# Kernel optimization log

Measured on AMD Instinct MI355X. Metric: run time of the kernel, lower is better.

Reference implementation:

```python
import jax, jax.numpy as jnp
import numpy as np

B, C, H, W = 2, 128, 64, 64
D_STATE = 16
EXPAND = 2
D_INNER = C * EXPAND          # 256
DT_RANK = -(-C // 16)         # 8
K = 4                         # scan directions
COMPRESS = 3
SQUEEZE = 30
EPS = 1e-5


def layernorm(x, g, b):
    mu = x.mean(-1, keepdims=True)
    xm = x - mu
    var = (xm * xm).mean(-1, keepdims=True)
    return xm * jax.lax.rsqrt(var + EPS) * g + b


def conv2d(x, w, bias, pad):
    y = jax.lax.conv_general_dilated(x, w, (1, 1), ((pad, pad), (pad, pad)),
                                     dimension_numbers=('NCHW', 'OIHW', 'NCHW'))
    return y + bias[None, :, None, None]


def selective_scan(xs, dts, A, Bs, Cs):
    # xs,dts: (B,K,D,L); A: (K,D,N); Bs,Cs: (B,K,N,L)
    dt_t = jnp.moveaxis(dts, -1, 0)
    x_t = jnp.moveaxis(xs, -1, 0)
    B_t = jnp.moveaxis(Bs, -1, 0)
    C_t = jnp.moveaxis(Cs, -1, 0)
    h0 = jnp.zeros(xs.shape[:3] + (A.shape[-1],), xs.dtype)

    def step(h, inp):
        dt_l, x_l, b_l, c_l = inp          # (B,K,D),(B,K,D),(B,K,N),(B,K,N)
        dA = jnp.exp(dt_l[..., None] * A)  # (B,K,D,N)
        h = dA * h + (dt_l * x_l)[..., None] * b_l[:, :, None, :]
        y = jnp.einsum('bkdn,bkn->bkd', h, c_l)
        return h, y

    _, ys = jax.lax.scan(step, h0, (dt_t, x_t, B_t, C_t))
    return jnp.moveaxis(ys, 0, -1)  # (B,K,D,L)


def ss2d(x, p):  # x: (B,H,W,C) -> (B,H,W,C)
    xz = x @ p['in_proj_w'].T
    xc, z = jnp.split(xz, 2, axis=-1)
    xc = xc.transpose(0, 3, 1, 2)  # (B,D,H,W)
    xc = jax.lax.conv_general_dilated(xc, p['conv_w'], (1, 1), ((1, 1), (1, 1)),
                                      feature_group_count=D_INNER,
                                      dimension_numbers=('NCHW', 'OIHW', 'NCHW'))
    xc = jax.nn.silu(xc + p['conv_b'][None, :, None, None])
    b, d, h, w = xc.shape
    L = h * w
    x_hw = xc.reshape(b, d, L)
    x_wh = xc.transpose(0, 1, 3, 2).reshape(b, d, L)
    xs = jnp.stack([x_hw, x_wh, x_hw[..., ::-1], x_wh[..., ::-1]], axis=1)  # (B,4,D,L)
    x_dbl = jnp.einsum('bkdl,kcd->bkcl', xs, p['x_proj_w'])
    dtr, Bs, Cs = jnp.split(x_dbl, [DT_RANK, DT_RANK + D_STATE], axis=2)
    dts = jnp.einsum('bkrl,kdr->bkdl', dtr, p['dt_w'])
    dts = jax.nn.softplus(dts + p['dt_b'][None, :, :, None])
    A = -jnp.exp(p['A_logs']).reshape(K, d, D_STATE)
    ys = selective_scan(xs, dts, A, Bs, Cs)
    ys = ys + xs * p['Ds'].reshape(K, d)[None, :, :, None]
    inv = ys[:, 2:4][..., ::-1]  # undo flipped scans
    wh = lambda t: t.reshape(b, d, w, h).transpose(0, 1, 3, 2).reshape(b, d, L)
    y = ys[:, 0] + inv[:, 0] + wh(ys[:, 1]) + wh(inv[:, 1])
    y = y.transpose(0, 2, 1).reshape(b, h, w, d)
    y = layernorm(y, p['out_norm_g'], p['out_norm_b'])
    y = y * jax.nn.silu(z)
    return y @ p['out_proj_w'].T


def cab(x, p):  # x: (B,C,H,W)
    t = jax.nn.gelu(conv2d(x, p['cab_w1'], p['cab_b1'], 1), approximate=False)
    t = conv2d(t, p['cab_w2'], p['cab_b2'], 1)
    s = t.mean((2, 3), keepdims=True)
    s = jax.nn.relu(conv2d(s, p['ca_w1'], p['ca_b1'], 0))
    s = jax.nn.sigmoid(conv2d(s, p['ca_w2'], p['ca_b2'], 0))
    return t * s


def vss_block(input, p):
    inp = input.transpose(0, 2, 3, 1)  # (B,H,W,C)
    x = inp * p['skip_scale'] + ss2d(layernorm(inp, p['ln1_g'], p['ln1_b']), p)
    c = cab(layernorm(x, p['ln2_g'], p['ln2_b']).transpose(0, 3, 1, 2), p)
    x = x * p['skip_scale2'] + c.transpose(0, 2, 3, 1)
    return x.transpose(0, 3, 1, 2)


def setup_inputs() -> dict:
    key = jax.random.key(0)
    ks = jax.random.split(key, 16)
    rn = lambda i, shp, s=0.02: jax.random.normal(ks[i], shp, jnp.float32) * s
    return {
        'input': jax.random.normal(ks[0], (B, C, H, W), jnp.float32),
        'ln1_g': jnp.ones((C,), jnp.float32), 'ln1_b': jnp.zeros((C,), jnp.float32),
        'skip_scale': jnp.ones((C,), jnp.float32), 'skip_scale2': jnp.ones((C,), jnp.float32),
        'ln2_g': jnp.ones((C,), jnp.float32), 'ln2_b': jnp.zeros((C,), jnp.float32),
        'in_proj_w': rn(1, (2 * D_INNER, C)),
        'conv_w': rn(2, (D_INNER, 1, 3, 3), 0.1),
        'conv_b': jnp.zeros((D_INNER,), jnp.float32),
        'x_proj_w': rn(3, (K, DT_RANK + 2 * D_STATE, D_INNER)),
        'dt_w': rn(4, (K, D_INNER, DT_RANK), 0.1),
        'dt_b': rn(5, (K, D_INNER), 0.1),
        'A_logs': jnp.log(jnp.tile(jnp.arange(1, D_STATE + 1, dtype=jnp.float32), (K * D_INNER, 1))),
        'Ds': jnp.ones((K * D_INNER,), jnp.float32),
        'out_norm_g': jnp.ones((D_INNER,), jnp.float32), 'out_norm_b': jnp.zeros((D_INNER,), jnp.float32),
        'out_proj_w': rn(6, (C, D_INNER)),
        'cab_w1': rn(7, (C // COMPRESS, C, 3, 3), 0.05),
        'cab_b1': jnp.zeros((C // COMPRESS,), jnp.float32),
        'cab_w2': rn(8, (C, C // COMPRESS, 3, 3), 0.05),
        'cab_b2': jnp.zeros((C,), jnp.float32),
        'ca_w1': rn(9, (C // SQUEEZE, C, 1, 1), 0.05),
        'ca_b1': jnp.zeros((C // SQUEEZE,), jnp.float32),
        'ca_w2': rn(10, (C, C // SQUEEZE, 1, 1), 0.05),
        'ca_b2': jnp.zeros((C,), jnp.float32),
    }


def reference(input, ln1_g, ln1_b, skip_scale, skip_scale2, ln2_g, ln2_b,
              in_proj_w, conv_w, conv_b, x_proj_w, dt_w, dt_b, A_logs, Ds,
              out_norm_g, out_norm_b, out_proj_w,
              cab_w1, cab_b1, cab_w2, cab_b2, ca_w1, ca_b1, ca_w2, ca_b2):
    p = dict(ln1_g=ln1_g, ln1_b=ln1_b, skip_scale=skip_scale, skip_scale2=skip_scale2,
             ln2_g=ln2_g, ln2_b=ln2_b, in_proj_w=in_proj_w, conv_w=conv_w, conv_b=conv_b,
             x_proj_w=x_proj_w, dt_w=dt_w, dt_b=dt_b, A_logs=A_logs, Ds=Ds,
             out_norm_g=out_norm_g, out_norm_b=out_norm_b, out_proj_w=out_proj_w,
             cab_w1=cab_w1, cab_b1=cab_b1, cab_w2=cab_w2, cab_b2=cab_b2,
             ca_w1=ca_w1, ca_b1=ca_b1, ca_w2=ca_w2, ca_b2=ca_b2)
    return vss_block(input, p)
```

## Files before the change

kernel.cpp:

```cpp
#include <hip/hip_runtime.h>
#include <math.h>

#define BB 2
#define CC 128
#define HH 64
#define WW 64
#define LL 4096
#define DI 256
#define NS 16
#define KK 4
#define OC1 42

#define NC 256
#define CL 16

#define K3_POS 16
#define BCW 48

__device__ __forceinline__ float sigmoidf_(float x) { return 1.f / (1.f + __expf(-x)); }
__device__ __forceinline__ float siluf_(float x)    { return x * sigmoidf_(x); }

__device__ __forceinline__ int scan_pos(int k, int i) {
  if (k == 0) return i;
  if (k == 1) return ((i & 63) << 6) | (i >> 6);
  if (k == 2) return (LL - 1) - i;
  int j = (LL - 1) - i;
  return ((j & 63) << 6) | (j >> 6);
}

__global__ __launch_bounds__(256) void k1_ln_inproj(
    const float* __restrict__ inp, const float* __restrict__ g, const float* __restrict__ b,
    const float* __restrict__ wproj, float* __restrict__ xcin, float* __restrict__ zbuf) {
  __shared__ float sx[64][132];
  __shared__ float sw[128][68];
  __shared__ float smu[64], srs[64];
  const int tid = threadIdx.x;
  const int rt = blockIdx.x & 3;
  const int pt = blockIdx.x >> 2;
  const int bb = pt >> 6;
  const int pbase = (pt & 63) << 6;

  for (int idx = tid; idx < 64 * CC; idx += 256) {
    int c = idx >> 6, pl = idx & 63;
    sx[pl][c] = inp[((size_t)bb * CC + c) * LL + pbase + pl];
  }
  __syncthreads();
  {
    int pl = tid >> 2, j = tid & 3;
    float s = 0.f, s2 = 0.f;
    for (int c = j; c < CC; c += 4) { float v = sx[pl][c]; s += v; s2 += v * v; }
    s += __shfl_xor(s, 1); s2 += __shfl_xor(s2, 1);
    s += __shfl_xor(s, 2); s2 += __shfl_xor(s2, 2);
    if (j == 0) {
      float mu = s * (1.f / CC);
      smu[pl] = mu;
      srs[pl] = rsqrtf(s2 * (1.f / CC) - mu * mu + 1e-5f);
    }
  }
  __syncthreads();
  for (int idx = tid; idx < 64 * CC; idx += 256) {
    int c = idx & 127, pl = idx >> 7;
    sx[pl][c] = (sx[pl][c] - smu[pl]) * srs[pl] * g[c] + b[c];
  }

  const int pg = tid & 7, rg = tid >> 3;
  float acc[8][4];
#pragma unroll
  for (int j = 0; j < 8; j++)
#pragma unroll
    for (int q = 0; q < 4; q++) acc[j][q] = 0.f;

  for (int kc = 0; kc < CC; kc += 64) {
    __syncthreads();
    for (int idx = tid; idx < 128 * 64; idx += 256) {
      int cl = idx & 63, rl = idx >> 6;
      sw[rl][cl] = wproj[(size_t)(rt * 128 + rl) * CC + kc + cl];
    }
    __syncthreads();
#pragma unroll 4
    for (int i = 0; i < 16; i++) {
      const int k0 = kc + 4 * i, kl0 = 4 * i;
      float4 xv[8], wv[4];
#pragma unroll
      for (int j = 0; j < 8; j++) xv[j] = *(const float4*)&sx[pg + 8 * j][k0];
#pragma unroll
      for (int q = 0; q < 4; q++) wv[q] = *(const float4*)&sw[rg + 32 * q][kl0];
#pragma unroll
      for (int j = 0; j < 8; j++)
#pragma unroll
        for (int q = 0; q < 4; q++) {
          acc[j][q] += xv[j].x * wv[q].x + xv[j].y * wv[q].y
                     + xv[j].z * wv[q].z + xv[j].w * wv[q].w;
        }
    }
  }

  float* buf = (rt < 2) ? xcin : zbuf;
  const int drow = (rt & 1) * 128;
#pragma unroll
  for (int j = 0; j < 8; j++) {
    const int p = pbase + pg + 8 * j;
    float* dst = buf + ((size_t)bb * LL + p) * DI + drow;
#pragma unroll
    for (int q = 0; q < 4; q++) dst[rg + 32 * q] = acc[j][q];
  }
}

__global__ __launch_bounds__(256) void k2_dwconv(
    const float* __restrict__ xcin, const float* __restrict__ cw, const float* __restrict__ cb,
    float* __restrict__ xconv) {
  const int w0 = (blockIdx.x & 7) * 8;
  const int hh = (blockIdx.x >> 3) & 63;
  const int bb = blockIdx.x >> 9;
  const int d = threadIdx.x;

  float wv[9];
#pragma unroll
  for (int kk = 0; kk < 9; kk++) wv[kk] = cw[d * 9 + kk];
  const float bias = cb[d];

  float xin[3][10];
#pragma unroll
  for (int kh = 0; kh < 3; kh++) {
    int r = hh + kh - 1;
    bool vr = (r >= 0 && r < HH);
#pragma unroll
    for (int c = 0; c < 10; c++) {
      int cc2 = w0 + c - 1;
      bool vc = (cc2 >= 0 && cc2 < WW);
      xin[kh][c] = (vr && vc) ? xcin[((size_t)bb * LL + r * WW + cc2) * DI + d] : 0.f;
    }
  }
#pragma unroll
  for (int j = 0; j < 8; j++) {
    float acc = bias;
#pragma unroll
    for (int kh = 0; kh < 3; kh++)
#pragma unroll
      for (int kw = 0; kw < 3; kw++)
        acc += wv[kh * 3 + kw] * xin[kh][j + kw];
    xconv[((size_t)bb * LL + hh * WW + w0 + j) * DI + d] = siluf_(acc);
  }
}

__global__ __launch_bounds__(256) void k3_proj(
    const float* __restrict__ xconv, const float* __restrict__ xpw,
    float* __restrict__ BCbuf) {
  __shared__ float sx[16][68];
  __shared__ float sw[160][68];
  const int tid = threadIdx.x;
  const int bb = blockIdx.x >> 8;
  const int pbase = (blockIdx.x & 255) << 4;

  const int pg = tid & 7, rb = tid >> 3;
  float acc[2][5];
#pragma unroll
  for (int j = 0; j < 2; j++)
#pragma unroll
    for (int q = 0; q < 5; q++) acc[j][q] = 0.f;

  for (int kc = 0; kc < DI; kc += 64) {
    __syncthreads();
    for (int idx = tid; idx < 16 * 64; idx += 256) {
      int cl = idx & 63, pl = idx >> 6;
      sx[pl][cl] = xconv[((size_t)bb * LL + pbase + pl) * DI + kc + cl];
    }
    for (int idx = tid; idx < 160 * 64; idx += 256) {
      int cl = idx & 63, rl = idx >> 6;
      sw[rl][cl] = xpw[(size_t)rl * DI + kc + cl];
    }
    __syncthreads();
#pragma unroll 4
    for (int i = 0; i < 16; i++) {
      float4 xv[2], wv[5];
#pragma unroll
      for (int j = 0; j < 2; j++) xv[j] = *(const float4*)&sx[2 * pg + j][4 * i];
#pragma unroll
      for (int q = 0; q < 5; q++) wv[q] = *(const float4*)&sw[rb + 32 * q][4 * i];
#pragma unroll
      for (int j = 0; j < 2; j++)
#pragma unroll
        for (int q = 0; q < 5; q++) {
          acc[j][q] += xv[j].x * wv[q].x + xv[j].y * wv[q].y
                     + xv[j].z * wv[q].z + xv[j].w * wv[q].w;
        }
    }
  }

#pragma unroll
  for (int j = 0; j < 2; j++) {
    const int p = pbase + 2 * pg + j;
#pragma unroll
    for (int q = 0; q < 5; q++) {
      const int r = rb + 32 * q;
      const int k = r / 40, c0 = r - k * 40;
      BCbuf[((size_t)(bb * KK + k) * LL + p) * BCW + c0] = acc[j][q];
    }
  }
}

__global__ __launch_bounds__(256) void k4a_chunk(
    const float* __restrict__ xconv, const float* __restrict__ BCbuf,
    const float* __restrict__ A_logs, const float* __restrict__ dtw,
    const float* __restrict__ dtb,
    float* __restrict__ csA, float* __restrict__ csB) {
  __shared__ float sBC[CL][26];
  const int d = threadIdx.x;
  const int chunk = blockIdx.x & (NC - 1);
  const int t = blockIdx.x / NC;
  const int k = t & 3;
  const int bb = t >> 2;
  const int bk = bb * KK + k;
  const int base = chunk * CL;

  for (int idx = d; idx < CL * 24; idx += 256) {
    int ii = idx / 24, j = idx - ii * 24;
    int pos = scan_pos(k, base + ii);
    sBC[ii][j] = BCbuf[((size_t)bk * LL + pos) * BCW + j];
  }
  float a[NS];
  bool fast = true;
#pragma unroll
  for (int n = 0; n < NS; n++) {
    a[n] = -__expf(A_logs[((size_t)k * DI + d) * NS + n]);
    fast = fast && (fabsf(a[n] + (float)(n + 1)) < 1e-3f * (n + 1));
  }
  const float* wdt = dtw + ((size_t)k * DI + d) * 8;
  const float4 wd0 = *(const float4*)wdt;
  const float4 wd1 = *(const float4*)(wdt + 4);
  const float bdt = dtb[k * DI + d];
  __syncthreads();

  const float* x_p = xconv + (size_t)bb * LL * DI + d;

  float Ap[NS], Bc[NS];
#pragma unroll
  for (int n = 0; n < NS; n++) { Ap[n] = 1.f; Bc[n] = 0.f; }

  if (fast) {
    float sumdt = 0.f;
#pragma unroll
    for (int half = 0; half < CL / 8; half++) {
      float xvr[8];
#pragma unroll
      for (int j = 0; j < 8; j++)
        xvr[j] = x_p[(size_t)scan_pos(k, base + half * 8 + j) * DI];
#pragma unroll
      for (int j = 0; j < 8; j++) {
        const int ii = half * 8 + j;
        const float* dr = sBC[ii];
        float u = bdt + wd0.x * dr[0] + wd0.y * dr[1] + wd0.z * dr[2] + wd0.w * dr[3]
                      + wd1.x * dr[4] + wd1.y * dr[5] + wd1.z * dr[6] + wd1.w * dr[7];
        float t2 = __expf(u);
        float E = __builtin_amdgcn_rcpf(1.f + t2);
        float dt = u > 20.f ? u : -0.69314718056f * __log2f(E);
        sumdt += dt;
        float dtx = dt * xvr[j];
        float E2 = E * E;
        float dA1 = E, dA2 = E2;
#pragma unroll
        for (int n = 0; n < NS; n += 2) {
          Bc[n] = dA1 * Bc[n] + dtx * sBC[ii][8 + n];
          Bc[n + 1] = dA2 * Bc[n + 1] + dtx * sBC[ii][9 + n];
          dA1 *= E2; dA2 *= E2;
        }
      }
    }
    float Et = __expf(-sumdt);
    float p = Et;
#pragma unroll
    for (int n = 0; n < NS; n++) { Ap[n] = p; p *= Et; }
  } else {
#pragma unroll 2
    for (int ii = 0; ii < CL; ii++) {
      int pos = scan_pos(k, base + ii);
      float xv = x_p[(size_t)pos * DI];
      const float* dr = sBC[ii];
      float u = bdt + wd0.x * dr[0] + wd0.y * dr[1] + wd0.z * dr[2] + wd0.w * dr[3]
                    + wd1.x * dr[4] + wd1.y * dr[5] + wd1.z * dr[6] + wd1.w * dr[7];
      float t2 = __expf(u);
      float dt = u > 20.f ? u : log1pf(t2);
      float dtx = dt * xv;
#pragma unroll
      for (int n = 0; n < NS; n++) {
        float dA = __expf(dt * a[n]);
        Ap[n] *= dA;
        Bc[n] = dA * Bc[n] + dtx * sBC[ii][8 + n];
      }
    }
  }
  size_t e = ((size_t)(bk * NC + chunk) * NS) * DI + d;
#pragma unroll
  for (int n = 0; n < NS; n++) {
    csA[e + (size_t)n * DI] = Ap[n];
    csB[e + (size_t)n * DI] = Bc[n];
  }
}

__global__ __launch_bounds__(256) void k4b_scanchunks(
    float* csAh, const float* __restrict__ csB) {
  const int d = threadIdx.x;
  const int n = blockIdx.x & (NS - 1);
  const int bk = blockIdx.x >> 4;
  const size_t stride = (size_t)NS * DI;
  size_t e = ((size_t)bk * NC * NS + n) * DI + d;
  float H = 0.f;
  for (int c0 = 0; c0 < NC; c0 += 16) {
    float A[16], Bv[16];
#pragma unroll
    for (int j = 0; j < 16; j++) {
      A[j]  = csAh[e + (size_t)j * stride];
      Bv[j] = csB[e + (size_t)j * stride];
    }
#pragma unroll
    for (int j = 0; j < 16; j++) {
      csAh[e + (size_t)j * stride] = H;
      H = A[j] * H + Bv[j];
    }
    e += (size_t)16 * stride;
  }
}

__global__ __launch_bounds__(256) void k4c_scan(
    const float* __restrict__ xconv, const float* __restrict__ BCbuf,
    const float* __restrict__ A_logs, const float* __restrict__ dtw,
    const float* __restrict__ dtb, const float* __restrict__ Ds,
    const float* __restrict__ hin, float* __restrict__ ys) {
  __shared__ float sBC[CL][BCW];
  const int d = threadIdx.x;
  const int chunk = blockIdx.x & (NC - 1);
  const int t = blockIdx.x / NC;
  const int k = t & 3;
  const int bb = t >> 2;
  const int bk = bb * KK + k;
  const int base = chunk * CL;

  for (int idx = d; idx < CL * 40; idx += 256) {
    int ii = idx / 40, j = idx - ii * 40;
    int pos = scan_pos(k, base + ii);
    sBC[ii][j] = BCbuf[((size_t)bk * LL + pos) * BCW + j];
  }
  float a[NS], h[NS];
  bool fast = true;
  const size_t eh = ((size_t)(bk * NC + chunk) * NS) * DI + d;
#pragma unroll
  for (int n = 0; n < NS; n++) {
    a[n] = -__expf(A_logs[((size_t)k * DI + d) * NS + n]);
    fast = fast && (fabsf(a[n] + (float)(n + 1)) < 1e-3f * (n + 1));
    h[n] = hin[eh + (size_t)n * DI];
  }
  const float* wdt = dtw + ((size_t)k * DI + d) * 8;
  const float4 wd0 = *(const float4*)wdt;
  const float4 wd1 = *(const float4*)(wdt + 4);
  const float bdt = dtb[k * DI + d];
  const float Dd = Ds[k * DI + d];
  __syncthreads();

  const float* x_p = xconv + (size_t)bb * LL * DI + d;
  float* ys_p = ys + (size_t)bk * LL * DI + d;

  if (fast) {
#pragma unroll
    for (int half = 0; half < CL / 8; half++) {
      float xvr[8];
#pragma unroll
      for (int j = 0; j < 8; j++)
        xvr[j] = x_p[(size_t)scan_pos(k, base + half * 8 + j) * DI];
#pragma unroll
      for (int j = 0; j < 8; j++) {
        const int ii = half * 8 + j;
        const float* dr = sBC[ii];
        float u = bdt + wd0.x * dr[0] + wd0.y * dr[1] + wd0.z * dr[2] + wd0.w * dr[3]
                      + wd1.x * dr[4] + wd1.y * dr[5] + wd1.z * dr[6] + wd1.w * dr[7];
        float t2 = __expf(u);
        float E = __builtin_amdgcn_rcpf(1.f + t2);
        float dt = u > 20.f ? u : -0.69314718056f * __log2f(E);
        float dtx = dt * xvr[j];
        float y = xvr[j] * Dd;
        float E2 = E * E;
        float dA1 = E, dA2 = E2;
#pragma unroll
        for (int n = 0; n < NS; n += 2) {
          h[n] = dA1 * h[n] + dtx * sBC[ii][8 + n];
          y += h[n] * sBC[ii][24 + n];
          h[n + 1] = dA2 * h[n + 1] + dtx * sBC[ii][9 + n];
          y += h[n + 1] * sBC[ii][25 + n];
          dA1 *= E2; dA2 *= E2;
        }
        ys_p[(size_t)scan_pos(k, base + ii) * DI] = y;
      }
    }
  } else {
#pragma unroll 2
    for (int ii = 0; ii < CL; ii++) {
      int pos = scan_pos(k, base + ii);
      float xv = x_p[(size_t)pos * DI];
      const float* dr = sBC[ii];
      float u = bdt + wd0.x * dr[0] + wd0.y * dr[1] + wd0.z * dr[2] + wd0.w * dr[3]
                    + wd1.x * dr[4] + wd1.y * dr[5] + wd1.z * dr[6] + wd1.w * dr[7];
      float t2 = __expf(u);
      float dt = u > 20.f ? u : log1pf(t2);
      float dtx = dt * xv;
      float y = xv * Dd;
#pragma unroll
      for (int n = 0; n < NS; n++) {
        float dA = __expf(dt * a[n]);
        h[n] = dA * h[n] + dtx * sBC[ii][8 + n];
        y += h[n] * sBC[ii][24 + n];
      }
      ys_p[(size_t)pos * DI] = y;
    }
  }
}

__global__ __launch_bounds__(256) void k5a_act(
    const float* __restrict__ ys, const float* __restrict__ zbuf,
    const float* __restrict__ ong, const float* __restrict__ onb,
    float* __restrict__ yact) {
  __shared__ float sy[8][260];
  __shared__ float smu[8], srs[8];
  const int tid = threadIdx.x;
  const int bb = blockIdx.x >> 9;
  const int pbase = (blockIdx.x & 511) << 3;

  for (int idx = tid; idx < 8 * DI; idx += 256) {
    int d = idx & 255, pl = idx >> 8;
    size_t o0 = (((size_t)bb * KK + 0) * LL + pbase + pl) * DI + d;
    const size_t st = (size_t)LL * DI;
    sy[pl][d] = ys[o0] + ys[o0 + st] + ys[o0 + 2 * st] + ys[o0 + 3 * st];
  }
  __syncthreads();
  {
    int pl = tid >> 5, j = tid & 31;
    float s = 0.f, s2 = 0.f;
    for (int d = j; d < DI; d += 32) { float v = sy[pl][d]; s += v; s2 += v * v; }
#pragma unroll
    for (int m = 1; m < 32; m <<= 1) { s += __shfl_xor(s, m); s2 += __shfl_xor(s2, m); }
    if (j == 0) {
      float mu = s * (1.f / DI);
      smu[pl] = mu;
      srs[pl] = rsqrtf(s2 * (1.f / DI) - mu * mu + 1e-5f);
    }
  }
  __syncthreads();
  for (int idx = tid; idx < 8 * DI; idx += 256) {
    int d = idx & 255, pl = idx >> 8;
    float zv = zbuf[((size_t)bb * LL + pbase + pl) * DI + d];
    yact[((size_t)bb * LL + pbase + pl) * DI + d] =
        ((sy[pl][d] - smu[pl]) * srs[pl] * ong[d] + onb[d]) * siluf_(zv);
  }
}

__global__ __launch_bounds__(256) void k5b_proj(
    const float* __restrict__ yact, const float* __restrict__ opw,
    const float* __restrict__ inp, const float* __restrict__ sk,
    const float* __restrict__ g2, const float* __restrict__ b2,
    float* __restrict__ xres, float* __restrict__ ln2) {
  __shared__ float sx[16][68];
  __shared__ float sw[128][68];
  __shared__ float sr[16][132];
  __shared__ float smu[16], srs[16];
  const int tid = threadIdx.x;
  const int bb = blockIdx.x >> 8;
  const int pbase = (blockIdx.x & 255) << 4;

  const int pg = tid & 7, rb = tid >> 3;
  float acc[2][4];
#pragma unroll
  for (int j = 0; j < 2; j++)
#pragma unroll
    for (int q = 0; q < 4; q++) acc[j][q] = 0.f;

  for (int kc = 0; kc < DI; kc += 64) {
    __syncthreads();
    for (int idx = tid; idx < 16 * 64; idx += 256) {
      int cl = idx & 63, pl = idx >> 6;
      sx[pl][cl] = yact[((size_t)bb * LL + pbase + pl) * DI + kc + cl];
    }
    for (int idx = tid; idx < 128 * 64; idx += 256) {
      int cl = idx & 63, rl = idx >> 6;
      sw[rl][cl] = opw[(size_t)rl * DI + kc + cl];
    }
    __syncthreads();
#pragma unroll 4
    for (int i = 0; i < 16; i++) {
      float4 xv[2], wv[4];
#pragma unroll
      for (int j = 0; j < 2; j++) xv[j] = *(const float4*)&sx[2 * pg + j][4 * i];
#pragma unroll
      for (int q = 0; q < 4; q++) wv[q] = *(const float4*)&sw[rb + 32 * q][4 * i];
#pragma unroll
      for (int j = 0; j < 2; j++)
#pragma unroll
        for (int q = 0; q < 4; q++) {
          acc[j][q] += xv[j].x * wv[q].x + xv[j].y * wv[q].y
                     + xv[j].z * wv[q].z + xv[j].w * wv[q].w;
        }
    }
  }

#pragma unroll
  for (int j = 0; j < 2; j++) {
    const int p = pbase + 2 * pg + j;
#pragma unroll
    for (int q = 0; q < 4; q++) {
      const int c = rb + 32 * q;
      float r = inp[((size_t)bb * CC + c) * LL + p] * sk[c] + acc[j][q];
      xres[((size_t)bb * LL + p) * CC + c] = r;
      sr[2 * pg + j][c] = r;
    }
  }
  __syncthreads();
  {
    int pl = tid >> 4, jj = tid & 15;
    float s = 0.f, s2 = 0.f;
    for (int c = jj; c < CC; c += 16) { float v = sr[pl][c]; s += v; s2 += v * v; }
#pragma unroll
    for (int m = 1; m < 16; m <<= 1) { s += __shfl_xor(s, m); s2 += __shfl_xor(s2, m); }
    if (jj == 0) {
      float mu = s * (1.f / CC);
      smu[pl] = mu;
      srs[pl] = rsqrtf(s2 * (1.f / CC) - mu * mu + 1e-5f);
    }
  }
  __syncthreads();
  for (int idx = tid; idx < 16 * CC; idx += 256) {
    int pl = idx & 15, c = idx >> 4;
    ln2[((size_t)bb * CC + c) * LL + pbase + pl] =
        (sr[pl][c] - smu[pl]) * srs[pl] * g2[c] + b2[c];
  }
}

__global__ __launch_bounds__(256) void k6a_conv1(
    const float* __restrict__ ln2, const float* __restrict__ w1,
    float* __restrict__ pc1) {
  __shared__ float sIn[16][6][68];
  __shared__ float sw[16 * 9 * OC1];
  const int tid = threadIdx.x;
  const int icq = blockIdx.x & 7;
  const int h4  = (blockIdx.x >> 3) & 15;
  const int bb  = blockIdx.x >> 7;
  const int icb = icq * 16;

  for (int idx = tid; idx < 16 * 6 * 66; idx += 256) {
    int i = idx / 396, rem = idx % 396;
    int rr = rem / 66, j = rem % 66;
    int r = h4 * 4 + rr - 1, c2 = j - 1;
    float v = 0.f;
    if (r >= 0 && r < HH && c2 >= 0 && c2 < WW)
      v = ln2[((size_t)bb * CC + icb + i) * LL + r * WW + c2];
    sIn[i][rr][j] = v;
  }
  for (int idx = tid; idx < OC1 * 16 * 9; idx += 256) {
    int oc = idx / 144, rem = idx % 144;
    int i = rem / 9, kk = rem % 9;
    sw[(i * 9 + kk) * OC1 + oc] = w1[((size_t)oc * CC + icb + i) * 9 + kk];
  }
  __syncthreads();

  const int wq = tid & 7, hq = (tid >> 3) & 3, ocg = tid >> 5;
  float acc[6][8];
#pragma unroll
  for (int q = 0; q < 6; q++)
#pragma unroll
    for (int ww = 0; ww < 8; ww++) acc[q][ww] = 0.f;

  for (int i = 0; i < 16; i++) {
    float xin[3][10];
#pragma unroll
    for (int kh = 0; kh < 3; kh++)
#pragma unroll
      for (int j = 0; j < 10; j++) xin[kh][j] = sIn[i][hq + kh][wq * 8 + j];
#pragma unroll
    for (int q = 0; q < 6; q++) {
      int oc = ocg + 8 * q;
      if (oc >= OC1) break;
      float wv[9];
#pragma unroll
      for (int kk = 0; kk < 9; kk++) wv[kk] = sw[(i * 9 + kk) * OC1 + oc];
#pragma unroll
      for (int kh = 0; kh < 3; kh++)
#pragma unroll
        for (int kw = 0; kw < 3; kw++)
#pragma unroll
          for (int ww = 0; ww < 8; ww++)
            acc[q][ww] += wv[kh * 3 + kw] * xin[kh][ww + kw];
    }
  }

  const int hrow = h4 * 4 + hq;
#pragma unroll
  for (int q = 0; q < 6; q++) {
    int oc = ocg + 8 * q;
    if (oc >= OC1) break;
    float* dst = pc1 + (((size_t)icq * BB + bb) * OC1 + oc) * LL + hrow * WW + wq * 8;
    *(float4*)dst       = make_float4(acc[q][0], acc[q][1], acc[q][2], acc[q][3]);
    *(float4*)(dst + 4) = make_float4(acc[q][4], acc[q][5], acc[q][6], acc[q][7]);
  }
}

__global__ __launch_bounds__(256) void k6b_reduce(
    const float* __restrict__ pc1, const float* __restrict__ b1,
    float* __restrict__ t1) {
  const int oc = blockIdx.x % OC1;
  const int bb = blockIdx.x / OC1;
  const float bias = b1[oc];
  const size_t st = (size_t)BB * OC1 * LL;
  const float* src = pc1 + ((size_t)bb * OC1 + oc) * LL;
  float* dst = t1 + ((size_t)bb * OC1 + oc) * LL;
  for (int i = threadIdx.x; i < LL / 4; i += 256) {
    float4 s = ((const float4*)src)[i];
#pragma unroll
    for (int icq = 1; icq < 8; icq++) {
      float4 v = *(const float4*)(src + (size_t)icq * st + i * 4);
      s.x += v.x; s.y += v.y; s.z += v.z; s.w += v.w;
    }
    float r[4] = {s.x + bias, s.y + bias, s.z + bias, s.w + bias};
#pragma unroll
    for (int q = 0; q < 4; q++)
      r[q] = 0.5f * r[q] * (1.f + erff(r[q] * 0.70710678118654752f));
    ((float4*)dst)[i] = make_float4(r[0], r[1], r[2], r[3]);
  }
}

__global__ __launch_bounds__(256) void k7_conv2(
    const float* __restrict__ t1, const float* __restrict__ w2,
    float* __restrict__ pc2) {
  __shared__ float sIn[21][4][68];
  __shared__ float swT[32 * 196];
  const int tid = threadIdx.x;
  const int icq = blockIdx.x & 1;
  const int h2  = (blockIdx.x >> 1) & 31;
  const int ocq = (blockIdx.x >> 6) & 3;
  const int bb  = blockIdx.x >> 8;
  const int icb = icq * 21;

  for (int idx = tid; idx < 21 * 4 * 66; idx += 256) {
    int i = idx / 264, rem = idx % 264;
    int rr = rem / 66, j = rem % 66;
    int r = h2 * 2 + rr - 1, c2 = j - 1;
    float v = 0.f;
    if (r >= 0 && r < HH && c2 >= 0 && c2 < WW)
      v = t1[((size_t)bb * OC1 + icb + i) * LL + r * WW + c2];
    sIn[i][rr][j] = v;
  }
  for (int idx = tid; idx < 32 * 189; idx += 256) {
    int ol = idx / 189, ikk = idx % 189;
    swT[ol * 196 + ikk] = w2[(size_t)(ocq * 32 + ol) * (OC1 * 9) + icb * 9 + ikk];
  }
  __syncthreads();

  const int wq = tid & 7, hq = (tid >> 3) & 1, ocg = tid >> 4;
  float acc[2][8];
#pragma unroll
  for (int q = 0; q < 2; q++)
#pragma unroll
    for (int ww = 0; ww < 8; ww++) acc[q][ww] = 0.f;

  for (int i = 0; i < 21; i++) {
    float xin[3][10];
#pragma unroll
    for (int kh = 0; kh < 3; kh++)
#pragma unroll
      for (int j = 0; j < 10; j++) xin[kh][j] = sIn[i][hq + kh][wq * 8 + j];
#pragma unroll
    for (int q = 0; q < 2; q++) {
      int ol = ocg + 16 * q;
      float wv[9];
#pragma unroll
      for (int kk = 0; kk < 9; kk++) wv[kk] = swT[ol * 196 + i * 9 + kk];
#pragma unroll
      for (int kh = 0; kh < 3; kh++)
#pragma unroll
        for (int kw = 0; kw < 3; kw++)
#pragma unroll
          for (int ww = 0; ww < 8; ww++)
            acc[q][ww] += wv[kh * 3 + kw] * xin[kh][ww + kw];
    }
  }

  const int hrow = h2 * 2 + hq;
#pragma unroll
  for (int q = 0; q < 2; q++) {
    int oc = ocq * 32 + ocg + 16 * q;
    float* dst = pc2 + (((size_t)icq * BB + bb) * CC + oc) * LL + hrow * WW + wq * 8;
    *(float4*)dst       = make_float4(acc[q][0], acc[q][1], acc[q][2], acc[q][3]);
    *(float4*)(dst + 4) = make_float4(acc[q][4], acc[q][5], acc[q][6], acc[q][7]);
  }
}

__global__ __launch_bounds__(256) void k8_mean(
    const float* __restrict__ pc2, const float* __restrict__ b2,
    float* __restrict__ t2, float* __restrict__ smean) {
  __shared__ float red[4];
  const int bc = blockIdx.x;
  const int bb = bc >> 7, c = bc & 127;
  const float bias = b2[c];
  const size_t st = (size_t)BB * CC * LL;
  const float* src = pc2 + ((size_t)bb * CC + c) * LL;
  float* dst = t2 + (size_t)bc * LL;
  float s = 0.f;
  for (int i = threadIdx.x; i < LL / 4; i += 256) {
    float4 v0 = ((const float4*)src)[i];
    float4 v1 = *(const float4*)(src + st + i * 4);
    float4 r = make_float4(v0.x + v1.x + bias, v0.y + v1.y + bias,
                           v0.z + v1.z + bias, v0.w + v1.w + bias);
    ((float4*)dst)[i] = r;
    s += r.x + r.y + r.z + r.w;
  }
#pragma unroll
  for (int m = 1; m < 64; m <<= 1) s += __shfl_xor(s, m);
  if ((threadIdx.x & 63) == 0) red[threadIdx.x >> 6] = s;
  __syncthreads();
  if (threadIdx.x == 0) smean[bc] = (red[0] + red[1] + red[2] + red[3]) * (1.f / LL);
}

__global__ __launch_bounds__(256) void k10_final(
    const float* __restrict__ xres, const float* __restrict__ t2,
    const float* __restrict__ smean,
    const float* __restrict__ cw1, const float* __restrict__ cb1,
    const float* __restrict__ cw2, const float* __restrict__ cb2,
    const float* __restrict__ sk2, float* __restrict__ out) {
  __shared__ float mid[4];
  const int tid = threadIdx.x;
  const int bc = blockIdx.x;
  const int bb = bc >> 7, c = bc & 127;

  {
    const int wv = tid >> 6, ln = tid & 63;
    float s = cw1[wv * CC + ln] * smean[bb * CC + ln]
            + cw1[wv * CC + 64 + ln] * smean[bb * CC + 64 + ln];
#pragma unroll
    for (int m = 1; m < 64; m <<= 1) s += __shfl_xor(s, m);
    if (ln == 0) mid[wv] = fmaxf(s + cb1[wv], 0.f);
  }
  __syncthreads();
  float a = cb2[c];
#pragma unroll
  for (int m = 0; m < 4; m++) a += cw2[c * 4 + m] * mid[m];
  const float sv = sigmoidf_(a);

  const float ss = sk2[c];
  const float* t2r = t2 + (size_t)bc * LL;
  float* outr = out + (size_t)bc * LL;
  for (int i = tid; i < LL; i += 256)
    outr[i] = xres[((size_t)bb * LL + i) * CC + c] * ss + t2r[i] * sv;
}


extern "C" void kernel_launch(void* const* d_in, const int* in_sizes, int n_in,
                              void* d_out, int out_size, void* d_ws, size_t ws_size,
                              hipStream_t stream) {
  const float* input      = (const float*)d_in[0];
  const float* ln1_g      = (const float*)d_in[1];
  const float* ln1_b      = (const float*)d_in[2];
  const float* skip_scale = (const float*)d_in[3];
  const float* skip_scale2= (const float*)d_in[4];
  const float* ln2_g      = (const float*)d_in[5];
  const float* ln2_b      = (const float*)d_in[6];
  const float* in_proj_w  = (const float*)d_in[7];
  const float* conv_w     = (const float*)d_in[8];
  const float* conv_b     = (const float*)d_in[9];
  const float* x_proj_w   = (const float*)d_in[10];
  const float* dt_w       = (const float*)d_in[11];
  const float* dt_b       = (const float*)d_in[12];
  const float* A_logs     = (const float*)d_in[13];
  const float* Ds         = (const float*)d_in[14];
  const float* out_norm_g = (const float*)d_in[15];
  const float* out_norm_b = (const float*)d_in[16];
  const float* out_proj_w = (const float*)d_in[17];
  const float* cab_w1     = (const float*)d_in[18];
  const float* cab_b1     = (const float*)d_in[19];
  const float* cab_w2     = (const float*)d_in[20];
  const float* cab_b2     = (const float*)d_in[21];
  const float* ca_w1      = (const float*)d_in[22];
  const float* ca_b1      = (const float*)d_in[23];
  const float* ca_w2      = (const float*)d_in[24];
  const float* ca_b2      = (const float*)d_in[25];

  float* ws = (float*)d_ws;
  float* xcin  = ws;
  float* zbuf  = xcin + (size_t)BB * LL * DI;
  float* xconv = zbuf + (size_t)BB * LL * DI;
  float* BCbuf = xconv + (size_t)BB * LL * DI;
  float* ysb   = BCbuf + (size_t)BB * KK * LL * BCW;
  float* xres  = ysb + (size_t)BB * KK * LL * DI;
  float* ln2b  = xres + (size_t)BB * LL * CC;
  float* t1b   = ln2b + (size_t)BB * CC * LL;
  float* t2b   = t1b + (size_t)BB * OC1 * LL;
  float* smean = t2b + (size_t)BB * CC * LL;
  float* csA   = smean + BB * CC;
  float* csB   = ysb;
  float* pc1   = ysb;
  float* yact  = csA;
  float* pc2   = ysb + (size_t)3 * 1024 * 1024;

  k1_ln_inproj<<<512, 256, 0, stream>>>(input, ln1_g, ln1_b, in_proj_w, xcin, zbuf);
  k2_dwconv<<<BB * HH * (WW / 8), 256, 0, stream>>>(xcin, conv_w, conv_b, xconv);
  k3_proj<<<BB * (LL / K3_POS), 256, 0, stream>>>(xconv, x_proj_w, BCbuf);
  k4a_chunk<<<BB * KK * NC, 256, 0, stream>>>(xconv, BCbuf, A_logs, dt_w, dt_b, csA, csB);
  k4b_scanchunks<<<BB * KK * NS, 256, 0, stream>>>(csA, csB);
  k4c_scan<<<BB * KK * NC, 256, 0, stream>>>(xconv, BCbuf, A_logs, dt_w, dt_b, Ds, csA, ysb);
  k5a_act<<<BB * (LL / 8), 256, 0, stream>>>(ysb, zbuf, out_norm_g, out_norm_b, yact);
  k5b_proj<<<BB * (LL / 16), 256, 0, stream>>>(yact, out_proj_w, input, skip_scale,
                                               ln2_g, ln2_b, xres, ln2b);
  k6a_conv1<<<BB * 16 * 8, 256, 0, stream>>>(ln2b, cab_w1, pc1);
  k6b_reduce<<<BB * OC1, 256, 0, stream>>>(pc1, cab_b1, t1b);
  k7_conv2<<<BB * 4 * 32 * 2, 256, 0, stream>>>(t1b, cab_w2, pc2);
  k8_mean<<<BB * CC, 256, 0, stream>>>(pc2, cab_b2, t2b, smean);
  k10_final<<<BB * CC, 256, 0, stream>>>(xres, t2b, smean, ca_w1, ca_b1, ca_w2, ca_b2,
                                         skip_scale2, (float*)d_out);
}
```

Baseline: 251.4 us.

## Store chunk dt sums instead of per-state decay and fuse out-norm into out_proj

The chunk pass now writes one summed dt per (chunk, channel) instead of 16 per-state decay products. The inter-chunk scan rebuilds each decay as exp(A*sumdt) on the fly and writes the carried states to a separate buffer. The layer norm plus SiLU gating stage is merged into the output projection kernel, so the activated tile stays in shared memory and the yact buffer round-trip and one launch go away. The cost is extra exp work in the serial chunk scan and more shared memory in the fused kernel, which may lower occupancy.

```diff
diff --git a/kernel.cpp b/kernel.cpp
--- a/kernel.cpp
+++ b/kernel.cpp
@@ -203,7 +203,7 @@
     const float* __restrict__ xconv, const float* __restrict__ BCbuf,
     const float* __restrict__ A_logs, const float* __restrict__ dtw,
     const float* __restrict__ dtb,
-    float* __restrict__ csA, float* __restrict__ csB) {
+    float* __restrict__ csS, float* __restrict__ csB) {
   __shared__ float sBC[CL][26];
   const int d = threadIdx.x;
   const int chunk = blockIdx.x & (NC - 1);
@@ -233,12 +233,12 @@
 
   const float* x_p = xconv + (size_t)bb * LL * DI + d;
 
-  float Ap[NS], Bc[NS];
-#pragma unroll
-  for (int n = 0; n < NS; n++) { Ap[n] = 1.f; Bc[n] = 0.f; }
+  float Bc[NS];
+#pragma unroll
+  for (int n = 0; n < NS; n++) Bc[n] = 0.f;
+  float sumdt = 0.f;
 
   if (fast) {
-    float sumdt = 0.f;
 #pragma unroll
     for (int half = 0; half < CL / 8; half++) {
       float xvr[8];
@@ -266,10 +266,6 @@
         }
       }
     }
-    float Et = __expf(-sumdt);
-    float p = Et;
-#pragma unroll
-    for (int n = 0; n < NS; n++) { Ap[n] = p; p *= Et; }
   } else {
 #pragma unroll 2
     for (int ii = 0; ii < CL; ii++) {
@@ -280,44 +276,48 @@
                     + wd1.x * dr[4] + wd1.y * dr[5] + wd1.z * dr[6] + wd1.w * dr[7];
       float t2 = __expf(u);
       float dt = u > 20.f ? u : log1pf(t2);
+      sumdt += dt;
       float dtx = dt * xv;
 #pragma unroll
       for (int n = 0; n < NS; n++) {
         float dA = __expf(dt * a[n]);
-        Ap[n] *= dA;
         Bc[n] = dA * Bc[n] + dtx * sBC[ii][8 + n];
       }
     }
   }
+  csS[((size_t)bk * NC + chunk) * DI + d] = sumdt;
   size_t e = ((size_t)(bk * NC + chunk) * NS) * DI + d;
 #pragma unroll
-  for (int n = 0; n < NS; n++) {
-    csA[e + (size_t)n * DI] = Ap[n];
+  for (int n = 0; n < NS; n++)
     csB[e + (size_t)n * DI] = Bc[n];
-  }
 }
 
 __global__ __launch_bounds__(256) void k4b_scanchunks(
-    float* csAh, const float* __restrict__ csB) {
+    const float* __restrict__ csS, const float* __restrict__ csB,
+    const float* __restrict__ A_logs, float* __restrict__ hin) {
   const int d = threadIdx.x;
   const int n = blockIdx.x & (NS - 1);
   const int bk = blockIdx.x >> 4;
-  const size_t stride = (size_t)NS * DI;
+  const int k = bk & 3;
+  const float an = -__expf(A_logs[((size_t)k * DI + d) * NS + n]);
+  const size_t strideB = (size_t)NS * DI;
   size_t e = ((size_t)bk * NC * NS + n) * DI + d;
   float H = 0.f;
   for (int c0 = 0; c0 < NC; c0 += 16) {
-    float A[16], Bv[16];
+    float Ea[16], Bv[16];
 #pragma unroll
     for (int j = 0; j < 16; j++) {
-      A[j]  = csAh[e + (size_t)j * stride];
-      Bv[j] = csB[e + (size_t)j * stride];
-    }
+      Ea[j] = an * csS[((size_t)bk * NC + c0 + j) * DI + d];
+      Bv[j] = csB[e + (size_t)j * strideB];
+    }
+#pragma unroll
+    for (int j = 0; j < 16; j++) Ea[j] = __expf(Ea[j]);
 #pragma unroll
     for (int j = 0; j < 16; j++) {
-      csAh[e + (size_t)j * stride] = H;
-      H = A[j] * H + Bv[j];
-    }
-    e += (size_t)16 * stride;
+      hin[e + (size_t)j * strideB] = H;
+      H = Ea[j] * H + Bv[j];
+    }
+    e += (size_t)16 * strideB;
   }
 }
 
@@ -413,50 +413,14 @@
   }
 }
 
-__global__ __launch_bounds__(256) void k5a_act(
+__global__ __launch_bounds__(256) void k5_fused(
     const float* __restrict__ ys, const float* __restrict__ zbuf,
     const float* __restrict__ ong, const float* __restrict__ onb,
-    float* __restrict__ yact) {
-  __shared__ float sy[8][260];
-  __shared__ float smu[8], srs[8];
-  const int tid = threadIdx.x;
-  const int bb = blockIdx.x >> 9;
-  const int pbase = (blockIdx.x & 511) << 3;
-
-  for (int idx = tid; idx < 8 * DI; idx += 256) {
-    int d = idx & 255, pl = idx >> 8;
-    size_t o0 = (((size_t)bb * KK + 0) * LL + pbase + pl) * DI + d;
-    const size_t st = (size_t)LL * DI;
-    sy[pl][d] = ys[o0] + ys[o0 + st] + ys[o0 + 2 * st] + ys[o0 + 3 * st];
-  }
-  __syncthreads();
-  {
-    int pl = tid >> 5, j = tid & 31;
-    float s = 0.f, s2 = 0.f;
-    for (int d = j; d < DI; d += 32) { float v = sy[pl][d]; s += v; s2 += v * v; }
-#pragma unroll
-    for (int m = 1; m < 32; m <<= 1) { s += __shfl_xor(s, m); s2 += __shfl_xor(s2, m); }
-    if (j == 0) {
-      float mu = s * (1.f / DI);
-      smu[pl] = mu;
-      srs[pl] = rsqrtf(s2 * (1.f / DI) - mu * mu + 1e-5f);
-    }
-  }
-  __syncthreads();
-  for (int idx = tid; idx < 8 * DI; idx += 256) {
-    int d = idx & 255, pl = idx >> 8;
-    float zv = zbuf[((size_t)bb * LL + pbase + pl) * DI + d];
-    yact[((size_t)bb * LL + pbase + pl) * DI + d] =
-        ((sy[pl][d] - smu[pl]) * srs[pl] * ong[d] + onb[d]) * siluf_(zv);
-  }
-}
-
-__global__ __launch_bounds__(256) void k5b_proj(
-    const float* __restrict__ yact, const float* __restrict__ opw,
+    const float* __restrict__ opw,
     const float* __restrict__ inp, const float* __restrict__ sk,
     const float* __restrict__ g2, const float* __restrict__ b2,
     float* __restrict__ xres, float* __restrict__ ln2) {
-  __shared__ float sx[16][68];
+  __shared__ float sy[16][260];
   __shared__ float sw[128][68];
   __shared__ float sr[16][132];
   __shared__ float smu[16], srs[16];
@@ -464,6 +428,32 @@
   const int bb = blockIdx.x >> 8;
   const int pbase = (blockIdx.x & 255) << 4;
 
+  for (int idx = tid; idx < 16 * DI; idx += 256) {
+    int d = idx & 255, pl = idx >> 8;
+    size_t o0 = (((size_t)bb * KK + 0) * LL + pbase + pl) * DI + d;
+    const size_t st = (size_t)LL * DI;
+    sy[pl][d] = ys[o0] + ys[o0 + st] + ys[o0 + 2 * st] + ys[o0 + 3 * st];
+  }
+  __syncthreads();
+  {
+    int pl = tid >> 4, j = tid & 15;
+    float s = 0.f, s2 = 0.f;
+    for (int d = j; d < DI; d += 16) { float v = sy[pl][d]; s += v; s2 += v * v; }
+#pragma unroll
+    for (int m = 1; m < 16; m <<= 1) { s += __shfl_xor(s, m); s2 += __shfl_xor(s2, m); }
+    if (j == 0) {
+      float mu = s * (1.f / DI);
+      smu[pl] = mu;
+      srs[pl] = rsqrtf(s2 * (1.f / DI) - mu * mu + 1e-5f);
+    }
+  }
+  __syncthreads();
+  for (int idx = tid; idx < 16 * DI; idx += 256) {
+    int d = idx & 255, pl = idx >> 8;
+    float zv = zbuf[((size_t)bb * LL + pbase + pl) * DI + d];
+    sy[pl][d] = ((sy[pl][d] - smu[pl]) * srs[pl] * ong[d] + onb[d]) * siluf_(zv);
+  }
+
   const int pg = tid & 7, rb = tid >> 3;
   float acc[2][4];
 #pragma unroll
@@ -473,10 +463,6 @@
 
   for (int kc = 0; kc < DI; kc += 64) {
     __syncthreads();
-    for (int idx = tid; idx < 16 * 64; idx += 256) {
-      int cl = idx & 63, pl = idx >> 6;
-      sx[pl][cl] = yact[((size_t)bb * LL + pbase + pl) * DI + kc + cl];
-    }
     for (int idx = tid; idx < 128 * 64; idx += 256) {
       int cl = idx & 63, rl = idx >> 6;
       sw[rl][cl] = opw[(size_t)rl * DI + kc + cl];
@@ -486,7 +472,7 @@
     for (int i = 0; i < 16; i++) {
       float4 xv[2], wv[4];
 #pragma unroll
-      for (int j = 0; j < 2; j++) xv[j] = *(const float4*)&sx[2 * pg + j][4 * i];
+      for (int j = 0; j < 2; j++) xv[j] = *(const float4*)&sy[2 * pg + j][kc + 4 * i];
 #pragma unroll
       for (int q = 0; q < 4; q++) wv[q] = *(const float4*)&sw[rb + 32 * q][4 * i];
 #pragma unroll
@@ -789,21 +775,20 @@
   float* t1b   = ln2b + (size_t)BB * CC * LL;
   float* t2b   = t1b + (size_t)BB * OC1 * LL;
   float* smean = t2b + (size_t)BB * CC * LL;
-  float* csA   = smean + BB * CC;
+  float* hinbuf= smean + BB * CC;
+  float* csS   = hinbuf + (size_t)BB * KK * NC * NS * DI;
   float* csB   = ysb;
   float* pc1   = ysb;
-  float* yact  = csA;
   float* pc2   = ysb + (size_t)3 * 1024 * 1024;
 
   k1_ln_inproj<<<512, 256, 0, stream>>>(input, ln1_g, ln1_b, in_proj_w, xcin, zbuf);
   k2_dwconv<<<BB * HH * (WW / 8), 256, 0, stream>>>(xcin, conv_w, conv_b, xconv);
   k3_proj<<<BB * (LL / K3_POS), 256, 0, stream>>>(xconv, x_proj_w, BCbuf);
-  k4a_chunk<<<BB * KK * NC, 256, 0, stream>>>(xconv, BCbuf, A_logs, dt_w, dt_b, csA, csB);
-  k4b_scanchunks<<<BB * KK * NS, 256, 0, stream>>>(csA, csB);
-  k4c_scan<<<BB * KK * NC, 256, 0, stream>>>(xconv, BCbuf, A_logs, dt_w, dt_b, Ds, csA, ysb);
-  k5a_act<<<BB * (LL / 8), 256, 0, stream>>>(ysb, zbuf, out_norm_g, out_norm_b, yact);
-  k5b_proj<<<BB * (LL / 16), 256, 0, stream>>>(yact, out_proj_w, input, skip_scale,
-                                               ln2_g, ln2_b, xres, ln2b);
+  k4a_chunk<<<BB * KK * NC, 256, 0, stream>>>(xconv, BCbuf, A_logs, dt_w, dt_b, csS, csB);
+  k4b_scanchunks<<<BB * KK * NS, 256, 0, stream>>>(csS, csB, A_logs, hinbuf);
+  k4c_scan<<<BB * KK * NC, 256, 0, stream>>>(xconv, BCbuf, A_logs, dt_w, dt_b, Ds, hinbuf, ysb);
+  k5_fused<<<BB * (LL / 16), 256, 0, stream>>>(ysb, zbuf, out_norm_g, out_norm_b, out_proj_w,
+                                               input, skip_scale, ln2_g, ln2_b, xres, ln2b);
   k6a_conv1<<<BB * 16 * 8, 256, 0, stream>>>(ln2b, cab_w1, pc1);
   k6b_reduce<<<BB * OC1, 256, 0, stream>>>(pc1, cab_b1, t1b);
   k7_conv2<<<BB * 4 * 32 * 2, 256, 0, stream>>>(t1b, cab_w2, pc2);
```

After: 246.4 us. 2.0% less time.
